# Kernel optimization log

Measured on AMD Instinct MI355X. Metric: run time of the kernel, lower is better.

Reference implementation:

```python
import math
import jax, jax.numpy as jnp
import numpy as np

TOP_K = 2
N_EXP = 8
TRAIN_CAPACITY = 1.25
MIN_CAPACITY = 4


def _capacity(num_tokens):
    cap = math.floor(TOP_K * TRAIN_CAPACITY * num_tokens / N_EXP)
    cap += cap % 2
    return max(cap, MIN_CAPACITY)


def _router(x, w_g):
    B, T, D = x.shape
    N = B * T
    C = _capacity(N)  # static: depends only on shapes

    logits = jnp.einsum('btd,ed->bte', x, w_g)            # [B,T,E]
    _, top_idx = jax.lax.top_k(logits, TOP_K)             # [B,T,K]
    probs = jax.nn.softmax(logits, axis=-1).reshape(N, N_EXP)  # [N,E]
    idx = top_idx.reshape(N, TOP_K)                       # [N,K]

    # one-hot expert mask, laid out [K, N, E] as in the torch code
    exp_mask = jax.nn.one_hot(idx, N_EXP, dtype=jnp.int32)      # [N,K,E]
    exp_mask = jnp.transpose(exp_mask, (1, 0, 2))               # [K,N,E]

    # position of each routed token within its expert's queue
    rank = jnp.cumsum(exp_mask.reshape(TOP_K * N, N_EXP), axis=0)
    rank = rank.reshape(TOP_K, N, N_EXP) - 1                    # [K,N,E]

    exp_mask = exp_mask * (rank < C).astype(jnp.int32)          # drop over-capacity
    used_capacity = jnp.sum(exp_mask, axis=(0, 1))              # [E]
    rank_sel = jnp.sum(exp_mask * rank, axis=-1)                # [K,N] int

    idx_kn = jnp.transpose(idx)                                 # [K,N]
    keep = jnp.take_along_axis(exp_mask, idx_kn[:, :, None], axis=2)[..., 0]  # [K,N]
    p_sel = jnp.transpose(jnp.take_along_axis(probs, idx, axis=1))            # [K,N]
    w = keep.astype(probs.dtype) * p_sel                        # [K,N]

    # cb_weight[n, e, c] = sum_k exp_weights[k,n,e] * one_hot(rank_sel)[k,n,c]
    # implemented as a direct scatter-add instead of materializing the
    # O(K*N*E*C) outer product (dropped tokens contribute weight 0).
    tok = jnp.arange(N)
    cb_weight = jnp.zeros((N, N_EXP, C), probs.dtype)
    cb_weight = cb_weight.at[tok[None, :], idx_kn, rank_sel].add(w)
    sec_mask = cb_weight != 0
    return used_capacity, cb_weight, sec_mask


def setup_inputs() -> dict:
    key = jax.random.key(0)
    kx, kw = jax.random.split(key)
    x = jax.random.normal(kx, (2, 2048, 1024), dtype=jnp.float32)
    w_g = jax.random.normal(kw, (8, 1024), dtype=jnp.float32) * 0.02
    return {"x": x, "w_g": w_g}


def reference(x, w_g):
    return _router(x, w_g)
```

## Files before the change

### kernel.cpp

```cpp
#include <hip/hip_runtime.h>

#define N_TOK 4096
#define DIM   1024
#define NE    8
#define CAP   1280
#define EC    (NE * CAP)
#define EC4   (EC / 4)
#define NEC   ((size_t)N_TOK * EC)

__global__ __launch_bounds__(256) void k_logits(const float* __restrict__ x,
                                                const float* __restrict__ wg,
                                                int* __restrict__ top_idx,
                                                float* __restrict__ top_p) {
    __shared__ float swg[NE * DIM];
    const float4* wg4 = (const float4*)wg;
    float4* swg4 = (float4*)swg;
#pragma unroll
    for (int i = 0; i < 8; ++i) {
        int t = i * 256 + threadIdx.x;
        swg4[t] = wg4[t];
    }
    __syncthreads();

    const int wave = threadIdx.x >> 6;
    const int lane = threadIdx.x & 63;
    const int token = blockIdx.x * 4 + wave;

    const float4* x4 = (const float4*)(x + (size_t)token * DIM);
    float acc[NE];
#pragma unroll
    for (int e = 0; e < NE; ++e) acc[e] = 0.f;

#pragma unroll
    for (int c = 0; c < 4; ++c) {
        float4 xv = x4[c * 64 + lane];
#pragma unroll
        for (int e = 0; e < NE; ++e) {
            float4 wv = swg4[e * 256 + c * 64 + lane];
            acc[e] += xv.x * wv.x + xv.y * wv.y + xv.z * wv.z + xv.w * wv.w;
        }
    }
#pragma unroll
    for (int e = 0; e < NE; ++e) {
        float v = acc[e];
#pragma unroll
        for (int off = 32; off > 0; off >>= 1)
            v += __shfl_xor(v, off, 64);
        acc[e] = v;
    }

    if (lane == 0) {
        float m = acc[0];
#pragma unroll
        for (int e = 1; e < NE; ++e) m = fmaxf(m, acc[e]);
        float pe[NE];
        float s = 0.f;
#pragma unroll
        for (int e = 0; e < NE; ++e) { pe[e] = expf(acc[e] - m); s += pe[e]; }
        float inv = 1.f / s;

        int i1 = 0; float v1 = acc[0];
#pragma unroll
        for (int e = 1; e < NE; ++e) if (acc[e] > v1) { v1 = acc[e]; i1 = e; }
        int i2 = (i1 == 0) ? 1 : 0; float v2 = acc[i2];
#pragma unroll
        for (int e = 0; e < NE; ++e)
            if (e != i1 && acc[e] > v2) { v2 = acc[e]; i2 = e; }

        top_idx[token]         = i1;
        top_idx[N_TOK + token] = i2;
        top_p[token]           = pe[i1] * inv;
        top_p[N_TOK + token]   = pe[i2] * inv;
    }
}

__global__ __launch_bounds__(64) void k_rank(const int* __restrict__ top_idx,
                                             const float* __restrict__ top_p,
                                             int* __restrict__ slot_tok,
                                             float* __restrict__ slot_w,
                                             float* __restrict__ used) {
    __shared__ int se[2 * N_TOK];
    const int lane = threadIdx.x;
    const int4* ti4 = (const int4*)top_idx;
    int4* se4 = (int4*)se;
#pragma unroll
    for (int i = 0; i < 32; ++i)
        se4[i * 64 + lane] = ti4[i * 64 + lane];
    __syncthreads();

    int cnt[NE];
#pragma unroll
    for (int e = 0; e < NE; ++e) cnt[e] = 0;
    const int base = lane * 128;
    for (int jj = 0; jj < 128; ++jj) cnt[se[base + jj]]++;

    int excl[NE], tot[NE];
#pragma unroll
    for (int e = 0; e < NE; ++e) {
        int v = cnt[e];
        int inc = v;
#pragma unroll
        for (int off = 1; off < 64; off <<= 1) {
            int u = __shfl_up(inc, off, 64);
            if (lane >= off) inc += u;
        }
        excl[e] = inc - v;
        tot[e] = __shfl(inc, 63, 64);
    }
    if (lane < NE) used[lane] = (float)min(tot[lane], CAP);

    int run[NE];
#pragma unroll
    for (int e = 0; e < NE; ++e) run[e] = excl[e];
    for (int jj = 0; jj < 128; ++jj) {
        int j = base + jj;
        int e = se[j];
        int r = run[e]++;
        if (r < CAP) {
            slot_tok[e * CAP + r] = j & (N_TOK - 1);
            slot_w[e * CAP + r]   = top_p[j];
        }
    }
#pragma unroll
    for (int e = 0; e < NE; ++e) {
        int start = min(tot[e], CAP);
        for (int s = start + lane; s < CAP; s += 64)
            slot_tok[e * CAP + s] = -1;
    }
}

__global__ __launch_bounds__(256) void k_out(const int* __restrict__ slot_tok,
                                             const float* __restrict__ slot_w,
                                             const float* __restrict__ used,
                                             float* __restrict__ out) {
    const int n = blockIdx.x;
    const int t = threadIdx.x;
    if (n == 0 && t < NE) out[t] = used[t];

    float4* cb = (float4*)(out + 8 + (size_t)n * EC);
    float4* mk = (float4*)(out + 8 + NEC + (size_t)n * EC);
    const int4* st4 = (const int4*)slot_tok;
    const float4* sw4 = (const float4*)slot_w;

#pragma unroll
    for (int i = 0; i < EC4 / 256; ++i) {
        int v = t + 256 * i;
        int4 tk = st4[v];
        float4 w = sw4[v];
        float4 c, m;
        c.x = (tk.x == n) ? w.x : 0.f;  m.x = (tk.x == n) ? 1.f : 0.f;
        c.y = (tk.y == n) ? w.y : 0.f;  m.y = (tk.y == n) ? 1.f : 0.f;
        c.z = (tk.z == n) ? w.z : 0.f;  m.z = (tk.z == n) ? 1.f : 0.f;
        c.w = (tk.w == n) ? w.w : 0.f;  m.w = (tk.w == n) ? 1.f : 0.f;
        cb[v] = c;
        mk[v] = m;
    }
}

extern "C" void kernel_launch(void* const* d_in, const int* in_sizes, int n_in,
                              void* d_out, int out_size, void* d_ws, size_t ws_size,
                              hipStream_t stream) {
    const float* x  = (const float*)d_in[0];
    const float* wg = (const float*)d_in[1];
    float* out = (float*)d_out;
    char* ws = (char*)d_ws;

    int*   top_idx  = (int*)(ws);
    float* top_p    = (float*)(ws + 32768);
    int*   slot_tok = (int*)(ws + 65536);
    float* slot_w   = (float*)(ws + 106496);
    float* used     = (float*)(ws + 147456);

    k_logits<<<N_TOK / 4, 256, 0, stream>>>(x, wg, top_idx, top_p);
    k_rank<<<1, 64, 0, stream>>>(top_idx, top_p, slot_tok, slot_w, used);
    k_out<<<N_TOK, 256, 0, stream>>>(slot_tok, slot_w, used, out);
}
```

Measured before the change: 391.9 us.

## Parallelize rank kernel across 256 threads and use nontemporal output stores

The single-block rank kernel grows from one wave to four. The token scan becomes a per-wave shuffle scan combined through shared-memory wave totals. Dynamic register-array indexing is replaced by unrolled select chains to avoid scratch spills. Separately, the large dense output writes in k_out now use nontemporal stores to reduce cache pollution on the write stream. The added block-level syncs and cross-wave offset logic add some complexity to the serial stage.

```diff
diff --git a/kernel.cpp b/kernel.cpp
--- a/kernel.cpp
+++ b/kernel.cpp
@@ -8,6 +8,8 @@
 #define EC4   (EC / 4)
 #define NEC   ((size_t)N_TOK * EC)
 
+typedef float nt_float4 __attribute__((ext_vector_type(4)));
+
 __global__ __launch_bounds__(256) void k_logits(const float* __restrict__ x,
                                                 const float* __restrict__ wg,
                                                 int* __restrict__ top_idx,
@@ -74,57 +76,90 @@
     }
 }
 
-__global__ __launch_bounds__(64) void k_rank(const int* __restrict__ top_idx,
-                                             const float* __restrict__ top_p,
-                                             int* __restrict__ slot_tok,
-                                             float* __restrict__ slot_w,
-                                             float* __restrict__ used) {
+__global__ __launch_bounds__(256) void k_rank(const int* __restrict__ top_idx,
+                                              const float* __restrict__ top_p,
+                                              int* __restrict__ slot_tok,
+                                              float* __restrict__ slot_w,
+                                              float* __restrict__ used) {
     __shared__ int se[2 * N_TOK];
-    const int lane = threadIdx.x;
+    __shared__ int wsum[4][NE];
+    __shared__ int s_start[NE];
+    const int t = threadIdx.x;
+    const int lane = t & 63;
+    const int wave = t >> 6;
+
     const int4* ti4 = (const int4*)top_idx;
     int4* se4 = (int4*)se;
 #pragma unroll
-    for (int i = 0; i < 32; ++i)
-        se4[i * 64 + lane] = ti4[i * 64 + lane];
+    for (int i = 0; i < 8; ++i)
+        se4[i * 256 + t] = ti4[i * 256 + t];
     __syncthreads();
 
     int cnt[NE];
 #pragma unroll
     for (int e = 0; e < NE; ++e) cnt[e] = 0;
-    const int base = lane * 128;
-    for (int jj = 0; jj < 128; ++jj) cnt[se[base + jj]]++;
-
-    int excl[NE], tot[NE];
-#pragma unroll
-    for (int e = 0; e < NE; ++e) {
-        int v = cnt[e];
-        int inc = v;
+    const int base = t * 32;
+#pragma unroll
+    for (int jj = 0; jj < 32; ++jj) {
+        int v = se[base + jj];
+#pragma unroll
+        for (int e = 0; e < NE; ++e) cnt[e] += (v == e) ? 1 : 0;
+    }
+
+    int incl[NE];
+#pragma unroll
+    for (int e = 0; e < NE; ++e) {
+        int s = cnt[e];
 #pragma unroll
         for (int off = 1; off < 64; off <<= 1) {
-            int u = __shfl_up(inc, off, 64);
-            if (lane >= off) inc += u;
-        }
-        excl[e] = inc - v;
-        tot[e] = __shfl(inc, 63, 64);
-    }
-    if (lane < NE) used[lane] = (float)min(tot[lane], CAP);
+            int u = __shfl_up(s, off, 64);
+            if (lane >= off) s += u;
+        }
+        incl[e] = s;
+        if (lane == 63) wsum[wave][e] = s;
+    }
+    __syncthreads();
+
+    int excl[NE];
+#pragma unroll
+    for (int e = 0; e < NE; ++e) {
+        int off = 0, total = 0;
+#pragma unroll
+        for (int w = 0; w < 4; ++w) {
+            int ws = wsum[w][e];
+            off   += (w < wave) ? ws : 0;
+            total += ws;
+        }
+        excl[e] = off + incl[e] - cnt[e];
+        if (t == 0) s_start[e] = min(total, CAP);
+    }
+    if (t < NE) {
+        int total = wsum[0][t] + wsum[1][t] + wsum[2][t] + wsum[3][t];
+        used[t] = (float)min(total, CAP);
+    }
 
     int run[NE];
 #pragma unroll
     for (int e = 0; e < NE; ++e) run[e] = excl[e];
-    for (int jj = 0; jj < 128; ++jj) {
+#pragma unroll
+    for (int jj = 0; jj < 32; ++jj) {
         int j = base + jj;
-        int e = se[j];
-        int r = run[e]++;
+        int v = se[j];
+        int r = run[0];
+#pragma unroll
+        for (int e = 1; e < NE; ++e) r = (v == e) ? run[e] : r;
+#pragma unroll
+        for (int e = 0; e < NE; ++e) run[e] += (v == e) ? 1 : 0;
         if (r < CAP) {
-            slot_tok[e * CAP + r] = j & (N_TOK - 1);
-            slot_w[e * CAP + r]   = top_p[j];
-        }
-    }
-#pragma unroll
-    for (int e = 0; e < NE; ++e) {
-        int start = min(tot[e], CAP);
-        for (int s = start + lane; s < CAP; s += 64)
+            slot_tok[v * CAP + r] = j & (N_TOK - 1);
+            slot_w[v * CAP + r]   = top_p[j];
+        }
+    }
+
+    __syncthreads();
+#pragma unroll
+    for (int e = 0; e < NE; ++e) {
+        for (int s = s_start[e] + t; s < CAP; s += 256)
             slot_tok[e * CAP + s] = -1;
     }
 }
@@ -137,8 +172,8 @@
     const int t = threadIdx.x;
     if (n == 0 && t < NE) out[t] = used[t];
 
-    float4* cb = (float4*)(out + 8 + (size_t)n * EC);
-    float4* mk = (float4*)(out + 8 + NEC + (size_t)n * EC);
+    nt_float4* cb = (nt_float4*)(out + 8 + (size_t)n * EC);
+    nt_float4* mk = (nt_float4*)(out + 8 + NEC + (size_t)n * EC);
     const int4* st4 = (const int4*)slot_tok;
     const float4* sw4 = (const float4*)slot_w;
 
@@ -147,13 +182,13 @@
         int v = t + 256 * i;
         int4 tk = st4[v];
         float4 w = sw4[v];
-        float4 c, m;
+        nt_float4 c, m;
         c.x = (tk.x == n) ? w.x : 0.f;  m.x = (tk.x == n) ? 1.f : 0.f;
         c.y = (tk.y == n) ? w.y : 0.f;  m.y = (tk.y == n) ? 1.f : 0.f;
         c.z = (tk.z == n) ? w.z : 0.f;  m.z = (tk.z == n) ? 1.f : 0.f;
         c.w = (tk.w == n) ? w.w : 0.f;  m.w = (tk.w == n) ? 1.f : 0.f;
-        cb[v] = c;
-        mk[v] = m;
+        __builtin_nontemporal_store(c, &cb[v]);
+        __builtin_nontemporal_store(m, &mk[v]);
     }
 }
 
@@ -172,6 +207,6 @@
     float* used     = (float*)(ws + 147456);
 
     k_logits<<<N_TOK / 4, 256, 0, stream>>>(x, wg, top_idx, top_p);
-    k_rank<<<1, 64, 0, stream>>>(top_idx, top_p, slot_tok, slot_w, used);
+    k_rank<<<1, 256, 0, stream>>>(top_idx, top_p, slot_tok, slot_w, used);
     k_out<<<N_TOK, 256, 0, stream>>>(slot_tok, slot_w, used, out);
 }
```

After: 394.3 us. Within noise of the previous version (+0.6%).
